# Kernel tuning notes

Measured on AMD Instinct MI355X. Metric: run time of the kernel, lower is better.

## Reference

```python
import jax, jax.numpy as jnp
import numpy as np

N_NODES = 50000
N_EDGES = 600000
IN_DIM = 128
HIDDEN = 128


def setup_inputs() -> dict:
    key = jax.random.key(0)
    k1, k2, k3, k4 = jax.random.split(key, 4)
    x = jax.random.normal(k1, (N_NODES, IN_DIM), dtype=jnp.float32)
    edge_index = jax.random.randint(k2, (2, N_EDGES), 0, N_NODES, dtype=jnp.int64)
    # Glorot-ish init for the two GCN layer weights
    W1 = jax.random.normal(k3, (IN_DIM, HIDDEN), dtype=jnp.float32) / np.sqrt(IN_DIM)
    b1 = jnp.zeros((HIDDEN,), dtype=jnp.float32)
    W2 = jax.random.normal(k4, (HIDDEN, HIDDEN), dtype=jnp.float32) / np.sqrt(HIDDEN)
    b2 = jnp.zeros((HIDDEN,), dtype=jnp.float32)
    return {"x": x, "edge_index": edge_index, "W1": W1, "b1": b1, "W2": W2, "b2": b2}


def _gcn_layer(x, W, b, src, dst, deg_inv_sqrt, n_nodes):
    # GCNConv: out = D^{-1/2} (A + I) D^{-1/2} X W + b, computed edge-wise.
    xw = x @ W                                           # [N, H] dense GEMM
    norm = deg_inv_sqrt[src] * deg_inv_sqrt[dst]         # [E+N]
    msg = xw[src] * norm[:, None]                        # gather + scale, [E+N, H]
    agg = jax.ops.segment_sum(msg, dst, num_segments=n_nodes)  # scatter-add
    return agg + b


def reference(x, edge_index, W1, b1, W2, b2):
    n_nodes = x.shape[0]
    loop = jnp.arange(n_nodes, dtype=edge_index.dtype)
    # add self-loops once; shared by both layers (same graph)
    src = jnp.concatenate([edge_index[0], loop])
    dst = jnp.concatenate([edge_index[1], loop])
    deg = jax.ops.segment_sum(jnp.ones_like(src, dtype=x.dtype), dst, num_segments=n_nodes)
    deg_inv_sqrt = jnp.where(deg > 0, jax.lax.rsqrt(jnp.maximum(deg, 1.0)), 0.0)

    h = jax.nn.relu(_gcn_layer(x, W1, b1, src, dst, deg_inv_sqrt, n_nodes))
    h = jax.nn.relu(_gcn_layer(h, W2, b2, src, dst, deg_inv_sqrt, n_nodes))
    return h
```

## Files before the change

### kernel.cpp

```cpp
#include <hip/hip_runtime.h>
#include <hip/hip_bf16.h>

#define DIM 128
#define CHUNK 4096
#define CAP 4096
typedef __hip_bfloat16 bf16;
typedef __attribute__((ext_vector_type(8))) short bf16x8;
typedef __attribute__((ext_vector_type(4))) float f32x4;

__global__ void prep_kernel(int* __restrict__ bcursor, int nbuck,
                            const int* __restrict__ ei, int E, int* __restrict__ misc,
                            const float* __restrict__ W1, const float* __restrict__ W2,
                            bf16* __restrict__ Wsw1, bf16* __restrict__ Wsw2) {
    if (blockIdx.x == 0) {
        for (int i = threadIdx.x; i < nbuck; i += 256) bcursor[i] = i * CAP;
    } else if (blockIdx.x == 1) {
        __shared__ int s_or;
        if (threadIdx.x == 0) s_or = 0;
        __syncthreads();
        int lim = E < 16384 ? E : 16384;
        int acc = 0;
        for (int j = threadIdx.x; j < lim; j += 256) acc |= ei[2 * j + 1];
        if (acc) atomicOr(&s_or, 1);
        __syncthreads();
        if (threadIdx.x == 0) misc[1] = s_or;
    } else {
        int id = (blockIdx.x - 2) * 256 + threadIdx.x;
        const float* W = (id < 2048) ? W1 : W2;
        bf16* Wsw = (id < 2048) ? Wsw1 : Wsw2;
        int t = id & 2047;
        int f = t >> 6, l = t & 63;
        int kt = f >> 3, nt = f & 7;
        int q = l >> 4, m = l & 15;
        bf16 tmp[8];
        #pragma unroll
        for (int j = 0; j < 8; ++j)
            tmp[j] = __float2bfloat16(W[(size_t)(kt * 32 + q * 8 + j) * DIM + nt * 16 + m]);
        *(bf16x8*)(Wsw + (size_t)t * 8) = *(const bf16x8*)tmp;
    }
}

template <bool XF32>
__device__ __forceinline__ void gemm_body(const void* __restrict__ Xv,
                                          const bf16* __restrict__ Wsw,
                                          bf16* __restrict__ Y, int N,
                                          int gw, int nw, int lane,
                                          float* sld) {
    int m = lane & 15, q = lane >> 4;
    const bf16x8* bp = (const bf16x8*)Wsw;
    for (int t = gw; t * 16 + 16 <= N; t += nw) {
        int base = t * 16;
        bf16x8 a[4];
        if (XF32) {
            const float* xp = (const float*)Xv + (size_t)(base + m) * DIM + q * 8;
            #pragma unroll
            for (int kt = 0; kt < 4; ++kt) {
                float4 v0 = *(const float4*)(xp + kt * 32);
                float4 v1 = *(const float4*)(xp + kt * 32 + 4);
                bf16 tt[8] = {__float2bfloat16(v0.x), __float2bfloat16(v0.y),
                              __float2bfloat16(v0.z), __float2bfloat16(v0.w),
                              __float2bfloat16(v1.x), __float2bfloat16(v1.y),
                              __float2bfloat16(v1.z), __float2bfloat16(v1.w)};
                a[kt] = *(const bf16x8*)tt;
            }
        } else {
            const bf16* xp = (const bf16*)Xv + (size_t)(base + m) * DIM + q * 8;
            #pragma unroll
            for (int kt = 0; kt < 4; ++kt)
                a[kt] = *(const bf16x8*)(xp + kt * 32);
        }
        f32x4 acc[8];
        #pragma unroll
        for (int nt = 0; nt < 8; ++nt) acc[nt] = (f32x4){0.f, 0.f, 0.f, 0.f};
        #pragma unroll
        for (int kt = 0; kt < 4; ++kt) {
            #pragma unroll
            for (int nt = 0; nt < 8; ++nt) {
                bf16x8 bfr = bp[(size_t)(kt * 8 + nt) * 64 + lane];
                acc[nt] = __builtin_amdgcn_mfma_f32_16x16x32_bf16(a[kt], bfr, acc[nt], 0, 0, 0);
            }
        }
        #pragma unroll
        for (int nt = 0; nt < 8; ++nt)
            #pragma unroll
            for (int r = 0; r < 4; ++r)
                sld[(q * 4 + r) * 132 + nt * 16 + m] = acc[nt][r];
        asm volatile("s_waitcnt lgkmcnt(0)" ::: "memory");
        #pragma unroll
        for (int i = 0; i < 4; ++i) {
            int row = i * 4 + q;
            const float* rp = sld + row * 132 + m * 8;
            float4 v0 = *(const float4*)rp;
            float4 v1 = *(const float4*)(rp + 4);
            alignas(16) bf16 tt[8] = {
                __float2bfloat16(v0.x), __float2bfloat16(v0.y),
                __float2bfloat16(v0.z), __float2bfloat16(v0.w),
                __float2bfloat16(v1.x), __float2bfloat16(v1.y),
                __float2bfloat16(v1.z), __float2bfloat16(v1.w)};
            *(uint4*)(Y + (size_t)(base + row) * DIM + m * 8) = *(const uint4*)tt;
        }
        asm volatile("s_waitcnt lgkmcnt(0)" ::: "memory");
    }
}

__global__ __launch_bounds__(256)
void scatter_gemm1(const int* __restrict__ ei, int E, const int* __restrict__ misc,
                   int* __restrict__ bcursor, unsigned* __restrict__ staged,
                   int nbuck, int nchunks,
                   const float* __restrict__ X, const bf16* __restrict__ Wsw,
                   bf16* __restrict__ Y, int N) {
    __shared__ float smem[4][16 * 132];
    int bx = blockIdx.x;
    if (bx < nchunks) {
        int* s_cnt  = (int*)&smem[0][0];
        int* s_base = s_cnt + 512;
        int* s_fill = s_cnt + 1024;
        for (int i = threadIdx.x; i < nbuck; i += 256) { s_cnt[i] = 0; s_fill[i] = 0; }
        __syncthreads();
        int flagI = misc[1];
        int c0 = bx * CHUNK;
        int cn = min(E - c0, CHUNK);
        for (int i = threadIdx.x; i < cn; i += 256) {
            int e = c0 + i;
            int d = (flagI == 0) ? ei[2 * E + 2 * e] : ei[E + e];
            atomicAdd(&s_cnt[d >> 7], 1);
        }
        __syncthreads();
        for (int i = threadIdx.x; i < nbuck; i += 256) {
            int c = s_cnt[i];
            s_base[i] = c ? atomicAdd(&bcursor[i], c) : 0;
        }
        __syncthreads();
        for (int i = threadIdx.x; i < cn; i += 256) {
            int e = c0 + i;
            int s, d;
            if (flagI == 0) { s = ei[2 * e]; d = ei[2 * E + 2 * e]; }
            else            { s = ei[e];     d = ei[E + e]; }
            int b = d >> 7;
            int r = s_base[b] + atomicAdd(&s_fill[b], 1);
            if (r < (b + 1) * CAP)
                staged[r] = ((unsigned)s << 7) | (unsigned)(d & 127);
        }
    } else {
        int wid = threadIdx.x >> 6, lane = threadIdx.x & 63;
        int ngw = (gridDim.x - nchunks) * 4;
        gemm_body<true>(X, Wsw, Y, N, (bx - nchunks) * 4 + wid, ngw, lane, smem[wid]);
    }
}

__global__ void bucket_sort(const unsigned* __restrict__ staged,
                            const int* __restrict__ bcursor,
                            int* __restrict__ csr, int* __restrict__ rowstart,
                            int* __restrict__ cnt, float* __restrict__ dis, int N) {
    __shared__ int s_cnt[128], s_off[128], s_fill[128], s_scan[128];
    int b = blockIdx.x, tid = threadIdx.x;
    int seg0 = b * CAP;
    int n = min(bcursor[b] - seg0, CAP);
    if (tid < 128) { s_cnt[tid] = 0; s_fill[tid] = 0; }
    __syncthreads();
    for (int i = tid; i < n; i += 256)
        atomicAdd(&s_cnt[staged[seg0 + i] & 127u], 1);
    __syncthreads();
    int v = (tid < 128) ? s_cnt[tid] : 0;
    if (tid < 128) s_scan[tid] = v;
    __syncthreads();
    for (int off = 1; off < 128; off <<= 1) {
        int t = (tid < 128 && tid >= off) ? s_scan[tid - off] : 0;
        __syncthreads();
        if (tid < 128) s_scan[tid] += t;
        __syncthreads();
    }
    if (tid < 128) {
        s_off[tid] = s_scan[tid] - v;
        int node = b * 128 + tid;
        if (node < N) {
            cnt[node] = v;
            rowstart[node] = seg0 + s_off[tid];
            dis[node] = rsqrtf((float)(v + 1));
        }
    }
    __syncthreads();
    for (int i = tid; i < n; i += 256) {
        unsigned p = staged[seg0 + i];
        int dl = p & 127u;
        int r = atomicAdd(&s_fill[dl], 1);
        csr[seg0 + s_off[dl] + r] = (int)(p >> 7);
    }
}

__device__ __forceinline__ void fma8(float* a, uint4 v, float ds) {
    a[0] = fmaf(__uint_as_float(v.x << 16), ds, a[0]);
    a[1] = fmaf(__uint_as_float(v.x & 0xffff0000u), ds, a[1]);
    a[2] = fmaf(__uint_as_float(v.y << 16), ds, a[2]);
    a[3] = fmaf(__uint_as_float(v.y & 0xffff0000u), ds, a[3]);
    a[4] = fmaf(__uint_as_float(v.z << 16), ds, a[4]);
    a[5] = fmaf(__uint_as_float(v.z & 0xffff0000u), ds, a[5]);
    a[6] = fmaf(__uint_as_float(v.w << 16), ds, a[6]);
    a[7] = fmaf(__uint_as_float(v.w & 0xffff0000u), ds, a[7]);
}

__device__ __forceinline__ void add8(float* a, uint4 v) {
    a[0] += __uint_as_float(v.x << 16);
    a[1] += __uint_as_float(v.x & 0xffff0000u);
    a[2] += __uint_as_float(v.y << 16);
    a[3] += __uint_as_float(v.y & 0xffff0000u);
    a[4] += __uint_as_float(v.z << 16);
    a[5] += __uint_as_float(v.z & 0xffff0000u);
    a[6] += __uint_as_float(v.w << 16);
    a[7] += __uint_as_float(v.w & 0xffff0000u);
}

__global__ __launch_bounds__(256, 4)
void agg1_gemm2(const uint4* __restrict__ Y, const int* __restrict__ rowstart,
                const int* __restrict__ cnt, const int* __restrict__ csr,
                const float* __restrict__ dis, const float* __restrict__ bias,
                const bf16* __restrict__ Wsw, bf16* __restrict__ Y2, int N) {
    __shared__ __align__(16) bf16 h_lds[16][136];
    __shared__ float s_out[16 * 132];
    int wave = threadIdx.x >> 6, lane = threadIdx.x & 63;
    int sub = lane >> 4, cl = lane & 15;
    int base = blockIdx.x * 16;
    int node = base + wave * 4 + sub;
    bool alive = node < N;

    float acc[4][8];
    #pragma unroll
    for (int j = 0; j < 4; ++j)
        #pragma unroll
        for (int k = 0; k < 8; ++k) acc[j][k] = 0.f;

    float dn = 0.f;
    if (alive) {
        int e0 = rowstart[node], e1 = e0 + cnt[node];
        dn = dis[node];
        fma8(acc[3], Y[(size_t)node * 16 + cl], dn);

        int e = e0;
        while (e + 8 <= e1) {
            int s[8];
            #pragma unroll
            for (int j = 0; j < 8; ++j) s[j] = csr[e + j];
            uint4 v[8]; float dv[8];
            #pragma unroll
            for (int j = 0; j < 8; ++j) { v[j] = Y[(size_t)s[j] * 16 + cl]; dv[j] = dis[s[j]]; }
            #pragma unroll
            for (int j = 0; j < 8; ++j) fma8(acc[j & 3], v[j], dv[j]);
            e += 8;
        }
        if (e + 4 <= e1) {
            int s[4];
            #pragma unroll
            for (int j = 0; j < 4; ++j) s[j] = csr[e + j];
            uint4 v[4]; float dv[4];
            #pragma unroll
            for (int j = 0; j < 4; ++j) { v[j] = Y[(size_t)s[j] * 16 + cl]; dv[j] = dis[s[j]]; }
            #pragma unroll
            for (int j = 0; j < 4; ++j) fma8(acc[j], v[j], dv[j]);
            e += 4;
        }
        for (; e < e1; ++e) {
            int s = csr[e];
            fma8(acc[0], Y[(size_t)s * 16 + cl], dis[s]);
        }
    }
    {
        float s8[8];
        #pragma unroll
        for (int k = 0; k < 8; ++k)
            s8[k] = (acc[0][k] + acc[1][k]) + (acc[2][k] + acc[3][k]);
        float4 b0 = ((const float4*)bias)[2 * cl];
        float4 b1 = ((const float4*)bias)[2 * cl + 1];
        alignas(16) bf16 t[8];
        t[0] = __float2bfloat16(alive ? fmaxf(dn * s8[0] + b0.x, 0.f) : 0.f);
        t[1] = __float2bfloat16(alive ? fmaxf(dn * s8[1] + b0.y, 0.f) : 0.f);
        t[2] = __float2bfloat16(alive ? fmaxf(dn * s8[2] + b0.z, 0.f) : 0.f);
        t[3] = __float2bfloat16(alive ? fmaxf(dn * s8[3] + b0.w, 0.f) : 0.f);
        t[4] = __float2bfloat16(alive ? fmaxf(dn * s8[4] + b1.x, 0.f) : 0.f);
        t[5] = __float2bfloat16(alive ? fmaxf(dn * s8[5] + b1.y, 0.f) : 0.f);
        t[6] = __float2bfloat16(alive ? fmaxf(dn * s8[6] + b1.z, 0.f) : 0.f);
        t[7] = __float2bfloat16(alive ? fmaxf(dn * s8[7] + b1.w, 0.f) : 0.f);
        *(uint4*)&h_lds[wave * 4 + sub][cl * 8] = *(const uint4*)t;
    }
    __syncthreads();

    int m = cl, q = sub;
    bf16x8 a[4];
    #pragma unroll
    for (int kt = 0; kt < 4; ++kt)
        a[kt] = *(const bf16x8*)&h_lds[m][q * 8 + kt * 32];
    const bf16x8* bp = (const bf16x8*)Wsw;
    f32x4 g[2];
    g[0] = (f32x4){0.f, 0.f, 0.f, 0.f};
    g[1] = (f32x4){0.f, 0.f, 0.f, 0.f};
    #pragma unroll
    for (int kt = 0; kt < 4; ++kt) {
        #pragma unroll
        for (int j = 0; j < 2; ++j) {
            int nt = wave * 2 + j;
            bf16x8 bfr = bp[(size_t)(kt * 8 + nt) * 64 + lane];
            g[j] = __builtin_amdgcn_mfma_f32_16x16x32_bf16(a[kt], bfr, g[j], 0, 0, 0);
        }
    }
    #pragma unroll
    for (int j = 0; j < 2; ++j)
        #pragma unroll
        for (int r = 0; r < 4; ++r)
            s_out[(q * 4 + r) * 132 + (wave * 2 + j) * 16 + m] = g[j][r];
    __syncthreads();

    int on = threadIdx.x >> 4;
    int oc = (threadIdx.x & 15) * 8;
    if (base + on < N) {
        float ds = dis[base + on];
        const float* rp = s_out + on * 132 + oc;
        float4 v0 = *(const float4*)rp;
        float4 v1 = *(const float4*)(rp + 4);
        alignas(16) bf16 t[8] = {
            __float2bfloat16(v0.x * ds), __float2bfloat16(v0.y * ds),
            __float2bfloat16(v0.z * ds), __float2bfloat16(v0.w * ds),
            __float2bfloat16(v1.x * ds), __float2bfloat16(v1.y * ds),
            __float2bfloat16(v1.z * ds), __float2bfloat16(v1.w * ds)};
        *(uint4*)(Y2 + (size_t)(base + on) * DIM + oc) = *(const uint4*)t;
    }
}

__global__ __launch_bounds__(256, 4)
void aggregate_final(const uint4* __restrict__ Y, const int* __restrict__ rowstart,
                     const int* __restrict__ cnt, const int* __restrict__ csr,
                     const float* __restrict__ dis, const float* __restrict__ bias,
                     float4* __restrict__ Of, int N) {
    int wave = threadIdx.x >> 6;
    int lane = threadIdx.x & 63;
    int sub = lane >> 4, cl = lane & 15;
    int node = blockIdx.x * 16 + wave * 4 + sub;
    if (node >= N) return;
    int e0 = rowstart[node], e1 = e0 + cnt[node];

    float acc[4][8];
    #pragma unroll
    for (int j = 0; j < 4; ++j)
        #pragma unroll
        for (int k = 0; k < 8; ++k) acc[j][k] = 0.f;

    float dn = dis[node];
    add8(acc[3], Y[(size_t)node * 16 + cl]);

    int e = e0;
    while (e + 8 <= e1) {
        int s[8];
        #pragma unroll
        for (int j = 0; j < 8; ++j) s[j] = csr[e + j];
        uint4 v[8];
        #pragma unroll
        for (int j = 0; j < 8; ++j) v[j] = Y[(size_t)s[j] * 16 + cl];
        #pragma unroll
        for (int j = 0; j < 8; ++j) add8(acc[j & 3], v[j]);
        e += 8;
    }
    if (e + 4 <= e1) {
        int s[4];
        #pragma unroll
        for (int j = 0; j < 4; ++j) s[j] = csr[e + j];
        uint4 v[4];
        #pragma unroll
        for (int j = 0; j < 4; ++j) v[j] = Y[(size_t)s[j] * 16 + cl];
        #pragma unroll
        for (int j = 0; j < 4; ++j) add8(acc[j], v[j]);
        e += 4;
    }
    for (; e < e1; ++e)
        add8(acc[0], Y[(size_t)csr[e] * 16 + cl]);

    float s8[8];
    #pragma unroll
    for (int k = 0; k < 8; ++k)
        s8[k] = (acc[0][k] + acc[1][k]) + (acc[2][k] + acc[3][k]);

    float4 b0 = ((const float4*)bias)[2 * cl];
    float4 b1 = ((const float4*)bias)[2 * cl + 1];
    float o[8];
    o[0] = fmaxf(dn * s8[0] + b0.x, 0.f);
    o[1] = fmaxf(dn * s8[1] + b0.y, 0.f);
    o[2] = fmaxf(dn * s8[2] + b0.z, 0.f);
    o[3] = fmaxf(dn * s8[3] + b0.w, 0.f);
    o[4] = fmaxf(dn * s8[4] + b1.x, 0.f);
    o[5] = fmaxf(dn * s8[5] + b1.y, 0.f);
    o[6] = fmaxf(dn * s8[6] + b1.z, 0.f);
    o[7] = fmaxf(dn * s8[7] + b1.w, 0.f);
    Of[(size_t)node * 32 + 2 * cl]     = make_float4(o[0], o[1], o[2], o[3]);
    Of[(size_t)node * 32 + 2 * cl + 1] = make_float4(o[4], o[5], o[6], o[7]);
}

extern "C" void kernel_launch(void* const* d_in, const int* in_sizes, int n_in,
                              void* d_out, int out_size, void* d_ws, size_t ws_size,
                              hipStream_t stream) {
    const float* x  = (const float*)d_in[0];
    const int*   ei = (const int*)d_in[1];
    const float* W1 = (const float*)d_in[2];
    const float* b1 = (const float*)d_in[3];
    const float* W2 = (const float*)d_in[4];
    const float* b2 = (const float*)d_in[5];

    int N = in_sizes[0] / DIM;
    int E = in_sizes[1] / 2;
    int nbuck = (N + 127) / 128;
    int nchunks = (E + CHUNK - 1) / CHUNK;

    char* w = (char*)d_ws;
    size_t used = 0;
    auto carve = [&](size_t bytes) {
        char* p = w + used;
        used += (bytes + 255) & ~(size_t)255;
        return p;
    };
    int*      misc     = (int*)     carve(256);
    int*      bcursor  = (int*)     carve((size_t)(nbuck + 1) * 4);
    unsigned* staged   = (unsigned*)carve((size_t)nbuck * CAP * 4);
    int*      csr      = (int*)     carve((size_t)nbuck * CAP * 4);
    int*      rowstart = (int*)     carve((size_t)N * 4);
    int*      cnt      = (int*)     carve((size_t)N * 4);
    float*    dis      = (float*)   carve((size_t)N * 4);
    bf16*     ybuf     = (bf16*)    carve((size_t)N * DIM * 2);
    bf16*     hbuf     = (bf16*)    carve((size_t)N * DIM * 2);
    bf16*     Wsw1     = (bf16*)    carve((size_t)DIM * DIM * 2);
    bf16*     Wsw2     = (bf16*)    carve((size_t)DIM * DIM * 2);

    prep_kernel <<<18, 256, 0, stream>>>(bcursor, nbuck, ei, E, misc, W1, W2, Wsw1, Wsw2);
    scatter_gemm1<<<nchunks + 784, 256, 0, stream>>>(ei, E, misc, bcursor, staged,
                                                     nbuck, nchunks, x, Wsw1, ybuf, N);
    bucket_sort <<<nbuck, 256, 0, stream>>>(staged, bcursor, csr, rowstart, cnt, dis, N);

    int ablocks = (N + 15) / 16;
    agg1_gemm2<<<ablocks, 256, 0, stream>>>((const uint4*)ybuf, rowstart, cnt, csr,
                                            dis, b1, Wsw2, hbuf, N);
    aggregate_final<<<ablocks, 256, 0, stream>>>((const uint4*)hbuf, rowstart, cnt, csr,
                                                 dis, b2, (float4*)d_out, N);
}
```

Measured before the change: 181.8 us.

## Keep W in registers for GEMM1, widen gather unroll, nontemporal output stores

The GEMM1 body now preloads all 32 swizzled weight fragments into registers once per wave instead of reloading them from global memory for every 16-row tile. The GEMM block count drops so each wave handles more tiles and amortizes that preload. The final aggregation adds a 12-wide gather loop for more memory-level parallelism, and the output is written with nontemporal stores. The costs are much higher VGPR pressure, with 128 extra registers for the weights, which can lower occupancy, plus fewer GEMM waves.

```diff
diff --git a/kernel.cpp b/kernel.cpp
--- a/kernel.cpp
+++ b/kernel.cpp
@@ -40,34 +40,29 @@
     }
 }
 
-template <bool XF32>
-__device__ __forceinline__ void gemm_body(const void* __restrict__ Xv,
+__device__ __forceinline__ void gemm_body(const float* __restrict__ Xv,
                                           const bf16* __restrict__ Wsw,
                                           bf16* __restrict__ Y, int N,
                                           int gw, int nw, int lane,
                                           float* sld) {
     int m = lane & 15, q = lane >> 4;
     const bf16x8* bp = (const bf16x8*)Wsw;
+    bf16x8 wreg[32];
+    #pragma unroll
+    for (int f = 0; f < 32; ++f) wreg[f] = bp[(size_t)f * 64 + lane];
     for (int t = gw; t * 16 + 16 <= N; t += nw) {
         int base = t * 16;
         bf16x8 a[4];
-        if (XF32) {
-            const float* xp = (const float*)Xv + (size_t)(base + m) * DIM + q * 8;
-            #pragma unroll
-            for (int kt = 0; kt < 4; ++kt) {
-                float4 v0 = *(const float4*)(xp + kt * 32);
-                float4 v1 = *(const float4*)(xp + kt * 32 + 4);
-                bf16 tt[8] = {__float2bfloat16(v0.x), __float2bfloat16(v0.y),
-                              __float2bfloat16(v0.z), __float2bfloat16(v0.w),
-                              __float2bfloat16(v1.x), __float2bfloat16(v1.y),
-                              __float2bfloat16(v1.z), __float2bfloat16(v1.w)};
-                a[kt] = *(const bf16x8*)tt;
-            }
-        } else {
-            const bf16* xp = (const bf16*)Xv + (size_t)(base + m) * DIM + q * 8;
-            #pragma unroll
-            for (int kt = 0; kt < 4; ++kt)
-                a[kt] = *(const bf16x8*)(xp + kt * 32);
+        const float* xp = Xv + (size_t)(base + m) * DIM + q * 8;
+        #pragma unroll
+        for (int kt = 0; kt < 4; ++kt) {
+            float4 v0 = *(const float4*)(xp + kt * 32);
+            float4 v1 = *(const float4*)(xp + kt * 32 + 4);
+            bf16 tt[8] = {__float2bfloat16(v0.x), __float2bfloat16(v0.y),
+                          __float2bfloat16(v0.z), __float2bfloat16(v0.w),
+                          __float2bfloat16(v1.x), __float2bfloat16(v1.y),
+                          __float2bfloat16(v1.z), __float2bfloat16(v1.w)};
+            a[kt] = *(const bf16x8*)tt;
         }
         f32x4 acc[8];
         #pragma unroll
@@ -75,10 +70,9 @@
         #pragma unroll
         for (int kt = 0; kt < 4; ++kt) {
             #pragma unroll
-            for (int nt = 0; nt < 8; ++nt) {
-                bf16x8 bfr = bp[(size_t)(kt * 8 + nt) * 64 + lane];
-                acc[nt] = __builtin_amdgcn_mfma_f32_16x16x32_bf16(a[kt], bfr, acc[nt], 0, 0, 0);
-            }
+            for (int nt = 0; nt < 8; ++nt)
+                acc[nt] = __builtin_amdgcn_mfma_f32_16x16x32_bf16(a[kt], wreg[kt * 8 + nt],
+                                                                  acc[nt], 0, 0, 0);
         }
         #pragma unroll
         for (int nt = 0; nt < 8; ++nt)
@@ -144,7 +138,7 @@
     } else {
         int wid = threadIdx.x >> 6, lane = threadIdx.x & 63;
         int ngw = (gridDim.x - nchunks) * 4;
-        gemm_body<true>(X, Wsw, Y, N, (bx - nchunks) * 4 + wid, ngw, lane, smem[wid]);
+        gemm_body(X, Wsw, Y, N, (bx - nchunks) * 4 + wid, ngw, lane, smem[wid]);
     }
 }
 
@@ -328,7 +322,7 @@
 void aggregate_final(const uint4* __restrict__ Y, const int* __restrict__ rowstart,
                      const int* __restrict__ cnt, const int* __restrict__ csr,
                      const float* __restrict__ dis, const float* __restrict__ bias,
-                     float4* __restrict__ Of, int N) {
+                     float* __restrict__ Of, int N) {
     int wave = threadIdx.x >> 6;
     int lane = threadIdx.x & 63;
     int sub = lane >> 4, cl = lane & 15;
@@ -346,7 +340,18 @@
     add8(acc[3], Y[(size_t)node * 16 + cl]);
 
     int e = e0;
-    while (e + 8 <= e1) {
+    while (e + 12 <= e1) {
+        int s[12];
+        #pragma unroll
+        for (int j = 0; j < 12; ++j) s[j] = csr[e + j];
+        uint4 v[12];
+        #pragma unroll
+        for (int j = 0; j < 12; ++j) v[j] = Y[(size_t)s[j] * 16 + cl];
+        #pragma unroll
+        for (int j = 0; j < 12; ++j) add8(acc[j & 3], v[j]);
+        e += 12;
+    }
+    if (e + 8 <= e1) {
         int s[8];
         #pragma unroll
         for (int j = 0; j < 8; ++j) s[j] = csr[e + j];
@@ -378,17 +383,18 @@
 
     float4 b0 = ((const float4*)bias)[2 * cl];
     float4 b1 = ((const float4*)bias)[2 * cl + 1];
-    float o[8];
-    o[0] = fmaxf(dn * s8[0] + b0.x, 0.f);
-    o[1] = fmaxf(dn * s8[1] + b0.y, 0.f);
-    o[2] = fmaxf(dn * s8[2] + b0.z, 0.f);
-    o[3] = fmaxf(dn * s8[3] + b0.w, 0.f);
-    o[4] = fmaxf(dn * s8[4] + b1.x, 0.f);
-    o[5] = fmaxf(dn * s8[5] + b1.y, 0.f);
-    o[6] = fmaxf(dn * s8[6] + b1.z, 0.f);
-    o[7] = fmaxf(dn * s8[7] + b1.w, 0.f);
-    Of[(size_t)node * 32 + 2 * cl]     = make_float4(o[0], o[1], o[2], o[3]);
-    Of[(size_t)node * 32 + 2 * cl + 1] = make_float4(o[4], o[5], o[6], o[7]);
+    f32x4 o0, o1;
+    o0[0] = fmaxf(dn * s8[0] + b0.x, 0.f);
+    o0[1] = fmaxf(dn * s8[1] + b0.y, 0.f);
+    o0[2] = fmaxf(dn * s8[2] + b0.z, 0.f);
+    o0[3] = fmaxf(dn * s8[3] + b0.w, 0.f);
+    o1[0] = fmaxf(dn * s8[4] + b1.x, 0.f);
+    o1[1] = fmaxf(dn * s8[5] + b1.y, 0.f);
+    o1[2] = fmaxf(dn * s8[6] + b1.z, 0.f);
+    o1[3] = fmaxf(dn * s8[7] + b1.w, 0.f);
+    f32x4* op = (f32x4*)(Of + (size_t)node * DIM + cl * 8);
+    __builtin_nontemporal_store(o0, op);
+    __builtin_nontemporal_store(o1, op + 1);
 }
 
 extern "C" void kernel_launch(void* const* d_in, const int* in_sizes, int n_in,
@@ -426,7 +432,7 @@
     bf16*     Wsw2     = (bf16*)    carve((size_t)DIM * DIM * 2);
 
     prep_kernel <<<18, 256, 0, stream>>>(bcursor, nbuck, ei, E, misc, W1, W2, Wsw1, Wsw2);
-    scatter_gemm1<<<nchunks + 784, 256, 0, stream>>>(ei, E, misc, bcursor, staged,
+    scatter_gemm1<<<nchunks + 196, 256, 0, stream>>>(ei, E, misc, bcursor, staged,
                                                      nbuck, nchunks, x, Wsw1, ybuf, N);
     bucket_sort <<<nbuck, 256, 0, stream>>>(staged, bcursor, csr, rowstart, cnt, dis, N);
 
@@ -434,5 +440,5 @@
     agg1_gemm2<<<ablocks, 256, 0, stream>>>((const uint4*)ybuf, rowstart, cnt, csr,
                                             dis, b1, Wsw2, hbuf, N);
     aggregate_final<<<ablocks, 256, 0, stream>>>((const uint4*)hbuf, rowstart, cnt, csr,
-                                                 dis, b2, (float4*)d_out, N);
-}
+                                                 dis, b2, (float*)d_out, N);
+}
```

Result: no change. 179.8 us (median of 2 runs) (-1.1%).
